# Kernel tuning notes

Measured on AMD Instinct MI355X. Metric: run time of the kernel, lower is better.

The kernel has to match this reference:

```python
import jax, jax.numpy as jnp
import numpy as np

NSTEPS = 20
ALPHA, BETA = 0.9, 0.85


def setup_inputs() -> dict:
    key = jax.random.key(0)
    ks = jax.random.split(key, 12)
    B, T, D_in, K, OUT = 64, NSTEPS, 16384, 25, 2
    dims = [8192, 4096, 2048]      # floor(dim/factor) per layer, factor=2
    prev = [16384, 8192, 4096]     # fan-in width each layer gathers from
    std = (2.0 / K) ** 0.5
    inp = {"x": jax.random.normal(ks[0], (B, T, D_in), jnp.float32)}
    for i, (d, p) in enumerate(zip(dims, prev)):
        inp[f"W{i}"] = jax.random.normal(ks[1 + i], (d, K), jnp.float32) * std
        inp[f"b{i}"] = jnp.zeros((1, d), jnp.float32)
        inp[f"knn{i}"] = jax.random.randint(ks[4 + i], (d, K), 0, p)
        inp[f"thr{i}"] = jax.random.uniform(ks[7 + i], (d,), jnp.float32)
    inp["Wfc"] = jax.random.normal(ks[10], (OUT, dims[-1]), jnp.float32) * dims[-1] ** -0.5
    inp["bfc"] = jnp.zeros((OUT,), jnp.float32)
    return inp


def reference(x, W0, b0, W1, b1, W2, b2, knn0, knn1, knn2,
              thr0, thr1, thr2, Wfc, bfc):
    # x: (B, T, D_in) -> scan over T
    Ws, bs = (W0, W1, W2), (b0, b1, b2)
    knns, thrs = (knn0, knn1, knn2), (thr0, thr1, thr2)
    n_layer = 3
    B = x.shape[0]
    xs = jnp.transpose(x, (1, 0, 2))  # (T, B, D_in)
    mems0 = tuple(jnp.zeros((B, w.shape[0]), x.dtype) for w in Ws)

    def step(mems, xt):
        h = xt
        new_mems, mem_recs, spk_recs = [], [], []
        for i in range(n_layer):
            g = h[:, knns[i]]                             # (B, dim_i, K) gather
            cur = jnp.einsum('bdk,dk->bd', g, Ws[i]) + bs[i]
            thr, mem_prev = thrs[i], mems[i]
            reset = (mem_prev > thr).astype(h.dtype)
            # NOTE: original code never writes the returned syn back, so the
            # synaptic state stays at zero init: syn = alpha*0 + cur = cur.
            syn = cur
            mem = BETA * mem_prev + syn - reset * thr
            spk = (mem - thr > 0).astype(h.dtype)
            if i == n_layer - 1:
                h = mem                 # last layer passes membrane forward
                new_mems.append(mem_prev)  # last-layer carry never updated
            else:
                h = spk
                new_mems.append(mem)
            mem_recs.append(mem)
            spk_recs.append(spk)
        angle = h @ Wfc.T + bfc
        return tuple(new_mems), (tuple(mem_recs), tuple(spk_recs), angle)

    _, (mem_rec, spk_rec, angles_all) = jax.lax.scan(step, mems0, xs)
    angles = angles_all[-1]  # original keeps only the last step's angle
    return (*mem_rec, *spk_rec, angles)
```

## Files before the change

kernel.cpp:

```cpp
#include <hip/hip_runtime.h>

#define NSTEPS 20
#define BATCH 64
#define D_IN 16384
#define KNN 25
#define BETA 0.85

#define D0 8192
#define D1 4096
#define D2 2048

#define NRT 24

__global__ void __launch_bounds__(256) transpose_x_kernel(
    const float* __restrict__ x, float* __restrict__ xT) {
  __shared__ float tile[64][65];
  const int t = blockIdx.y;
  const int d0 = blockIdx.x * 64;
  {
    const int dd = threadIdx.x & 63;
    const int bg = threadIdx.x >> 6;
#pragma unroll
    for (int i = 0; i < 16; ++i) {
      const int b = bg * 16 + i;
      tile[b][dd] = x[((size_t)b * NSTEPS + t) * D_IN + d0 + dd];
    }
  }
  __syncthreads();
  {
    const int b = threadIdx.x & 63;
    const int dg = threadIdx.x >> 6;
#pragma unroll
    for (int i = 0; i < 16; ++i) {
      const int d = dg * 16 + i;
      xT[((size_t)t * D_IN + d0 + d) * BATCH + b] = tile[b][d];
    }
  }
}

template <bool IS_U8>
__global__ void __launch_bounds__(512) cur_kernel(
    const void* __restrict__ src, size_t st_t, const float* __restrict__ W,
    const float* __restrict__ bias, const int* __restrict__ knn, int dn,
    int dchunk0, double* __restrict__ curbuf) {
  const int nb_d = dn >> 4;
  const int g = blockIdx.x & 7;
  const int q = blockIdx.x >> 3;
  const int r = q / nb_d;
  const int i = q - r * nb_d;
  const int t = r * 8 + g;
  if (t >= NSTEPS) return;

  const int lane = threadIdx.x & 63;
  const int wv = threadIdx.x >> 6;
  const int dl0 = i * 16 + wv * 2;

  double cc[2];
#pragma unroll
  for (int j = 0; j < 2; ++j) {
    const int dl = dl0 + j;
    const int dg = __builtin_amdgcn_readfirstlane(dchunk0 + dl);
    const int* kp = knn + (size_t)dg * KNN;
    const float* wp = W + (size_t)dg * KNN;
    double cur = (double)bias[dg];
    if (IS_U8) {
      const unsigned char* sp =
          (const unsigned char*)src + (size_t)t * st_t + lane;
#pragma unroll
      for (int k = 0; k < KNN; ++k) {
        const int idx = kp[k];
        cur += (double)wp[k] * (double)sp[(size_t)idx * BATCH];
      }
    } else {
      const float* sp = (const float*)src + (size_t)t * st_t + lane;
#pragma unroll
      for (int k = 0; k < KNN; ++k) {
        const int idx = kp[k];
        cur += (double)wp[k] * (double)sp[(size_t)idx * BATCH];
      }
    }
    cc[j] = cur;
  }
  double2 v;
  v.x = cc[0];
  v.y = cc[1];
  const size_t o =
      (((size_t)t * (dn >> 1) + (dl0 >> 1)) * BATCH + lane) * 2;
  *reinterpret_cast<double2*>(&curbuf[o]) = v;
}

__global__ void __launch_bounds__(512) scan_kernel(
    const double* __restrict__ curbuf, int dn, int dchunk0, int D,
    const float* __restrict__ thr, float* __restrict__ mem_rec,
    float* __restrict__ spk_rec, unsigned char* __restrict__ spkT) {
  __shared__ float s_mem[16][68];
  __shared__ float s_spk[16][68];
  const int dl0 = blockIdx.x * 16;
  const int lane = threadIdx.x & 63;
  const int wv = threadIdx.x >> 6;
  const int dbase = dl0 + wv * 2;

  double mem[2] = {0.0, 0.0};
  double thrv[2];
#pragma unroll
  for (int j = 0; j < 2; ++j) thrv[j] = (double)thr[dchunk0 + dbase + j];

  for (int t = 0; t < NSTEPS; ++t) {
    const double2 cc = *reinterpret_cast<const double2*>(
        &curbuf[(((size_t)t * (dn >> 1) + (dbase >> 1)) * BATCH + lane) * 2]);
#pragma unroll
    for (int j = 0; j < 2; ++j) {
      const int dl = dbase + j;
      const double cur = (j == 0) ? cc.x : cc.y;
      double m = mem[j];
      const double reset = (m > thrv[j]) ? thrv[j] : 0.0;
      m = BETA * m + cur - reset;
      mem[j] = m;
      const float spk = (m > thrv[j]) ? 1.0f : 0.0f;
      s_mem[wv * 2 + j][lane] = (float)m;
      s_spk[wv * 2 + j][lane] = spk;
      if (spkT)
        spkT[((size_t)t * D + dchunk0 + dl) * BATCH + lane] =
            (unsigned char)spk;
    }
    __syncthreads();
    {
      const int b = threadIdx.x & 63;
      const int q = threadIdx.x >> 6;
      const int dq = (q & 3) * 4;
      const float(*sp)[68] = (q < 4) ? s_mem : s_spk;
      float4 v;
      v.x = sp[dq + 0][b];
      v.y = sp[dq + 1][b];
      v.z = sp[dq + 2][b];
      v.w = sp[dq + 3][b];
      float* dst = (q < 4) ? mem_rec : spk_rec;
      const size_t o = ((size_t)t * BATCH + b) * D + dchunk0 + dl0 + dq;
      *reinterpret_cast<float4*>(&dst[o]) = v;
    }
    __syncthreads();
  }
}

template <bool IS_U8, bool CARRY>
__global__ void __launch_bounds__(512) layer_scan_kernel(
    const void* __restrict__ src, size_t st_t, size_t st_b, size_t st_idx,
    const float* __restrict__ W, const float* __restrict__ bias,
    const int* __restrict__ knn, const float* __restrict__ thr, int D,
    float* __restrict__ mem_rec, float* __restrict__ spk_rec,
    unsigned char* __restrict__ spkT) {
  __shared__ float s_mem[16][68];
  __shared__ float s_spk[16][68];
  const int d0 = blockIdx.x * 16;
  const int lane = threadIdx.x & 63;
  const int wv = threadIdx.x >> 6;
  const int dbase = d0 + wv * 2;

  double mem[2] = {0.0, 0.0};
  double thrv[2], bsv[2];
#pragma unroll
  for (int j = 0; j < 2; ++j) {
    thrv[j] = (double)thr[dbase + j];
    bsv[j] = (double)bias[dbase + j];
  }

  const int t_lo = CARRY ? 0 : (int)blockIdx.y;
  const int t_hi = CARRY ? NSTEPS : (int)blockIdx.y + 1;

  for (int t = t_lo; t < t_hi; ++t) {
#pragma unroll
    for (int j = 0; j < 2; ++j) {
      const int d = dbase + j;
      const int* kp = knn + (size_t)d * KNN;
      const float* wp = W + (size_t)d * KNN;
      const size_t base = (size_t)t * st_t + (size_t)lane * st_b;
      double cur = bsv[j];
#pragma unroll
      for (int k = 0; k < KNN; ++k) {
        const int idx = kp[k];
        if (IS_U8) {
          const unsigned char s =
              ((const unsigned char*)src)[base + (size_t)idx * st_idx];
          cur += (double)wp[k] * (double)s;
        } else {
          const float g = ((const float*)src)[base + (size_t)idx * st_idx];
          cur += (double)wp[k] * (double)g;
        }
      }
      double m = CARRY ? mem[j] : 0.0;
      const double reset = (m > thrv[j]) ? thrv[j] : 0.0;
      m = BETA * m + cur - reset;
      mem[j] = m;
      const float spk = (m > thrv[j]) ? 1.0f : 0.0f;
      s_mem[wv * 2 + j][lane] = (float)m;
      s_spk[wv * 2 + j][lane] = spk;
      if (spkT) spkT[((size_t)t * D + d) * BATCH + lane] = (unsigned char)spk;
    }
    __syncthreads();
    {
      const int b = threadIdx.x & 63;
      const int q = threadIdx.x >> 6;
      const int dq = (q & 3) * 4;
      const float(*sp)[68] = (q < 4) ? s_mem : s_spk;
      float4 v;
      v.x = sp[dq + 0][b];
      v.y = sp[dq + 1][b];
      v.z = sp[dq + 2][b];
      v.w = sp[dq + 3][b];
      float* dst = (q < 4) ? mem_rec : spk_rec;
      const size_t o = ((size_t)t * BATCH + b) * D + d0 + dq;
      *reinterpret_cast<float4*>(&dst[o]) = v;
    }
    __syncthreads();
  }
}

__global__ void __launch_bounds__(64) fc_kernel(
    const float* __restrict__ mem2, const float* __restrict__ Wfc,
    const float* __restrict__ bfc, float* __restrict__ angles) {
  const int b = blockIdx.x;
  const float* h = mem2 + ((size_t)(NSTEPS - 1) * BATCH + b) * D2;
  double a0 = 0.0, a1 = 0.0;
  for (int d = threadIdx.x; d < D2; d += 64) {
    const double m = (double)h[d];
    a0 += m * (double)Wfc[d];
    a1 += m * (double)Wfc[D2 + d];
  }
#pragma unroll
  for (int off = 32; off > 0; off >>= 1) {
    a0 += __shfl_down(a0, off);
    a1 += __shfl_down(a1, off);
  }
  if (threadIdx.x == 0) {
    angles[(size_t)b * 2 + 0] = (float)(a0 + (double)bfc[0]);
    angles[(size_t)b * 2 + 1] = (float)(a1 + (double)bfc[1]);
  }
}

extern "C" void kernel_launch(void* const* d_in, const int* in_sizes, int n_in,
                              void* d_out, int out_size, void* d_ws,
                              size_t ws_size, hipStream_t stream) {
  const float* x = (const float*)d_in[0];
  const float* W0 = (const float*)d_in[1];
  const float* b0 = (const float*)d_in[2];
  const int* knn0 = (const int*)d_in[3];
  const float* thr0 = (const float*)d_in[4];
  const float* W1 = (const float*)d_in[5];
  const float* b1 = (const float*)d_in[6];
  const int* knn1 = (const int*)d_in[7];
  const float* thr1 = (const float*)d_in[8];
  const float* W2 = (const float*)d_in[9];
  const float* b2 = (const float*)d_in[10];
  const int* knn2 = (const int*)d_in[11];
  const float* thr2 = (const float*)d_in[12];
  const float* Wfc = (const float*)d_in[13];
  const float* bfc = (const float*)d_in[14];

  float* out = (float*)d_out;
  float* mem_rec0 = out;
  float* mem_rec1 = mem_rec0 + (size_t)NSTEPS * BATCH * D0;
  float* mem_rec2 = mem_rec1 + (size_t)NSTEPS * BATCH * D1;
  float* spk_rec0 = mem_rec2 + (size_t)NSTEPS * BATCH * D2;
  float* spk_rec1 = spk_rec0 + (size_t)NSTEPS * BATCH * D0;
  float* spk_rec2 = spk_rec1 + (size_t)NSTEPS * BATCH * D1;
  float* angles = spk_rec2 + (size_t)NSTEPS * BATCH * D2;

  const size_t xT_bytes = (size_t)NSTEPS * D_IN * BATCH * sizeof(float);
  const size_t s0_bytes = (size_t)NSTEPS * D0 * BATCH;
  const size_t s1_bytes = (size_t)NSTEPS * D1 * BATCH;
  const size_t base_bytes = xT_bytes + s0_bytes + s1_bytes;

  const bool planA = ws_size >= base_bytes;
  const bool planB = !planA && ws_size >= s0_bytes + s1_bytes;

  size_t leftover = (ws_size > base_bytes) ? ws_size - base_bytes : 0;
  int Dc = (int)((leftover / ((size_t)NSTEPS * BATCH * 8)) & ~(size_t)15);
  if (Dc > D0) Dc = D0;
  const bool planT = planA && Dc >= 512;

  const dim3 blk(512);

  if (planT) {
    float* xT = (float*)d_ws;
    unsigned char* spk0T = (unsigned char*)d_ws + xT_bytes;
    unsigned char* spk1T = spk0T + s0_bytes;
    double* curbuf = (double*)((char*)d_ws + base_bytes);

    transpose_x_kernel<<<dim3(D_IN / 64, NSTEPS), 256, 0, stream>>>(x, xT);

    for (int c0 = 0; c0 < D0; c0 += Dc) {
      const int dn = (D0 - c0 < Dc) ? (D0 - c0) : Dc;
      cur_kernel<false><<<dim3(NRT * (dn / 16)), blk, 0, stream>>>(
          xT, (size_t)D_IN * BATCH, W0, b0, knn0, dn, c0, curbuf);
      scan_kernel<<<dim3(dn / 16), blk, 0, stream>>>(
          curbuf, dn, c0, D0, thr0, mem_rec0, spk_rec0, spk0T);
    }
    for (int c0 = 0; c0 < D1; c0 += Dc) {
      const int dn = (D1 - c0 < Dc) ? (D1 - c0) : Dc;
      cur_kernel<true><<<dim3(NRT * (dn / 16)), blk, 0, stream>>>(
          spk0T, (size_t)D0 * BATCH, W1, b1, knn1, dn, c0, curbuf);
      scan_kernel<<<dim3(dn / 16), blk, 0, stream>>>(
          curbuf, dn, c0, D1, thr1, mem_rec1, spk_rec1, spk1T);
    }
    layer_scan_kernel<true, false><<<dim3(D2 / 16, NSTEPS), blk, 0, stream>>>(
        spk1T, (size_t)D1 * BATCH, 1, BATCH, W2, b2, knn2, thr2, D2, mem_rec2,
        spk_rec2, nullptr);
  } else if (planA) {
    float* xT = (float*)d_ws;
    unsigned char* spk0T = (unsigned char*)d_ws + xT_bytes;
    unsigned char* spk1T = spk0T + s0_bytes;

    transpose_x_kernel<<<dim3(D_IN / 64, NSTEPS), 256, 0, stream>>>(x, xT);
    layer_scan_kernel<false, true><<<dim3(D0 / 16), blk, 0, stream>>>(
        xT, (size_t)D_IN * BATCH, 1, BATCH, W0, b0, knn0, thr0, D0, mem_rec0,
        spk_rec0, spk0T);
    layer_scan_kernel<true, true><<<dim3(D1 / 16), blk, 0, stream>>>(
        spk0T, (size_t)D0 * BATCH, 1, BATCH, W1, b1, knn1, thr1, D1, mem_rec1,
        spk_rec1, spk1T);
    layer_scan_kernel<true, false><<<dim3(D2 / 16, NSTEPS), blk, 0, stream>>>(
        spk1T, (size_t)D1 * BATCH, 1, BATCH, W2, b2, knn2, thr2, D2, mem_rec2,
        spk_rec2, nullptr);
  } else if (planB) {
    unsigned char* spk0T = (unsigned char*)d_ws;
    unsigned char* spk1T = spk0T + s0_bytes;

    layer_scan_kernel<false, true><<<dim3(D0 / 16), blk, 0, stream>>>(
        x, (size_t)D_IN, (size_t)NSTEPS * D_IN, 1, W0, b0, knn0, thr0, D0,
        mem_rec0, spk_rec0, spk0T);
    layer_scan_kernel<true, true><<<dim3(D1 / 16), blk, 0, stream>>>(
        spk0T, (size_t)D0 * BATCH, 1, BATCH, W1, b1, knn1, thr1, D1, mem_rec1,
        spk_rec1, spk1T);
    layer_scan_kernel<true, false><<<dim3(D2 / 16, NSTEPS), blk, 0, stream>>>(
        spk1T, (size_t)D1 * BATCH, 1, BATCH, W2, b2, knn2, thr2, D2, mem_rec2,
        spk_rec2, nullptr);
  } else {
    layer_scan_kernel<false, true><<<dim3(D0 / 16), blk, 0, stream>>>(
        x, (size_t)D_IN, (size_t)NSTEPS * D_IN, 1, W0, b0, knn0, thr0, D0,
        mem_rec0, spk_rec0, nullptr);
    layer_scan_kernel<false, true><<<dim3(D1 / 16), blk, 0, stream>>>(
        spk_rec0, (size_t)BATCH * D0, (size_t)D0, 1, W1, b1, knn1, thr1, D1,
        mem_rec1, spk_rec1, nullptr);
    layer_scan_kernel<false, false><<<dim3(D2 / 16, NSTEPS), blk, 0, stream>>>(
        spk_rec1, (size_t)BATCH * D1, (size_t)D1, 1, W2, b2, knn2, thr2, D2,
        mem_rec2, spk_rec2, nullptr);
  }

  fc_kernel<<<dim3(BATCH), 64, 0, stream>>>(mem_rec2, Wfc, bfc, angles);
}
```

Baseline: 249.5 us.

## Compact cur_kernel grid mapping and shrink scan blocks with two-step batching

The cur_kernel grid no longer launches 24 time-slots per d-block, of which 4 exit immediately. It now packs exactly NSTEPS*nb_d work items into 8 contiguous XCD-style groups, so each group gets a contiguous run of (t, d-block) items. scan_kernel drops to 256 threads covering 8 neurons, which doubles its block count for better occupancy. Each iteration now handles two timesteps, halving the barrier count and issuing both curbuf loads up front. The trade-off is more shared-memory staging per iteration and a changed block-to-XCD locality pattern.

Result: slower. 277.4 us (+11.2%).

```diff
diff --git a/kernel.cpp b/kernel.cpp
--- a/kernel.cpp
+++ b/kernel.cpp
@@ -9,8 +9,6 @@
 #define D0 8192
 #define D1 4096
 #define D2 2048
-
-#define NRT 24
 
 __global__ void __launch_bounds__(256) transpose_x_kernel(
     const float* __restrict__ x, float* __restrict__ xT) {
@@ -43,13 +41,15 @@
     const void* __restrict__ src, size_t st_t, const float* __restrict__ W,
     const float* __restrict__ bias, const int* __restrict__ knn, int dn,
     int dchunk0, double* __restrict__ curbuf) {
-  const int nb_d = dn >> 4;
-  const int g = blockIdx.x & 7;
-  const int q = blockIdx.x >> 3;
-  const int r = q / nb_d;
-  const int i = q - r * nb_d;
-  const int t = r * 8 + g;
-  if (t >= NSTEPS) return;
+  const unsigned nb_d = (unsigned)dn >> 4;
+  const unsigned Wk = NSTEPS * nb_d;
+  const unsigned C = (Wk + 7u) >> 3;
+  const unsigned g = blockIdx.x & 7u;
+  const unsigned s = blockIdx.x >> 3;
+  const unsigned u = g * C + s;
+  if (s >= C || u >= Wk) return;
+  const int t = (int)(u / nb_d);
+  const int i = (int)(u - (unsigned)t * nb_d);
 
   const int lane = threadIdx.x & 63;
   const int wv = threadIdx.x >> 6;
@@ -84,18 +84,17 @@
   double2 v;
   v.x = cc[0];
   v.y = cc[1];
-  const size_t o =
-      (((size_t)t * (dn >> 1) + (dl0 >> 1)) * BATCH + lane) * 2;
+  const size_t o = (((size_t)t * (dn >> 1) + (dl0 >> 1)) * BATCH + lane) * 2;
   *reinterpret_cast<double2*>(&curbuf[o]) = v;
 }
 
-__global__ void __launch_bounds__(512) scan_kernel(
+__global__ void __launch_bounds__(256) scan_kernel(
     const double* __restrict__ curbuf, int dn, int dchunk0, int D,
     const float* __restrict__ thr, float* __restrict__ mem_rec,
     float* __restrict__ spk_rec, unsigned char* __restrict__ spkT) {
-  __shared__ float s_mem[16][68];
-  __shared__ float s_spk[16][68];
-  const int dl0 = blockIdx.x * 16;
+  __shared__ float s_mem[2][8][68];
+  __shared__ float s_spk[2][8][68];
+  const int dl0 = blockIdx.x * 8;
   const int lane = threadIdx.x & 63;
   const int wv = threadIdx.x >> 6;
   const int dbase = dl0 + wv * 2;
@@ -105,38 +104,50 @@
 #pragma unroll
   for (int j = 0; j < 2; ++j) thrv[j] = (double)thr[dchunk0 + dbase + j];
 
-  for (int t = 0; t < NSTEPS; ++t) {
-    const double2 cc = *reinterpret_cast<const double2*>(
-        &curbuf[(((size_t)t * (dn >> 1) + (dbase >> 1)) * BATCH + lane) * 2]);
-#pragma unroll
-    for (int j = 0; j < 2; ++j) {
-      const int dl = dbase + j;
-      const double cur = (j == 0) ? cc.x : cc.y;
-      double m = mem[j];
-      const double reset = (m > thrv[j]) ? thrv[j] : 0.0;
-      m = BETA * m + cur - reset;
-      mem[j] = m;
-      const float spk = (m > thrv[j]) ? 1.0f : 0.0f;
-      s_mem[wv * 2 + j][lane] = (float)m;
-      s_spk[wv * 2 + j][lane] = spk;
-      if (spkT)
-        spkT[((size_t)t * D + dchunk0 + dl) * BATCH + lane] =
-            (unsigned char)spk;
+  const size_t row = (size_t)(dn >> 1);
+  for (int t0 = 0; t0 < NSTEPS; t0 += 2) {
+    const double2 c0 = *reinterpret_cast<const double2*>(
+        &curbuf[(((size_t)t0 * row + (dbase >> 1)) * BATCH + lane) * 2]);
+    const double2 c1 = *reinterpret_cast<const double2*>(
+        &curbuf[(((size_t)(t0 + 1) * row + (dbase >> 1)) * BATCH + lane) * 2]);
+#pragma unroll
+    for (int tt = 0; tt < 2; ++tt) {
+      const double2 cc = tt ? c1 : c0;
+      const int t = t0 + tt;
+#pragma unroll
+      for (int j = 0; j < 2; ++j) {
+        const int dl = dbase + j;
+        const double cur = (j == 0) ? cc.x : cc.y;
+        double m = mem[j];
+        const double reset = (m > thrv[j]) ? thrv[j] : 0.0;
+        m = BETA * m + cur - reset;
+        mem[j] = m;
+        const float spk = (m > thrv[j]) ? 1.0f : 0.0f;
+        s_mem[tt][wv * 2 + j][lane] = (float)m;
+        s_spk[tt][wv * 2 + j][lane] = spk;
+        if (spkT)
+          spkT[((size_t)t * D + dchunk0 + dl) * BATCH + lane] =
+              (unsigned char)spk;
+      }
     }
     __syncthreads();
     {
       const int b = threadIdx.x & 63;
       const int q = threadIdx.x >> 6;
-      const int dq = (q & 3) * 4;
-      const float(*sp)[68] = (q < 4) ? s_mem : s_spk;
-      float4 v;
-      v.x = sp[dq + 0][b];
-      v.y = sp[dq + 1][b];
-      v.z = sp[dq + 2][b];
-      v.w = sp[dq + 3][b];
-      float* dst = (q < 4) ? mem_rec : spk_rec;
-      const size_t o = ((size_t)t * BATCH + b) * D + dchunk0 + dl0 + dq;
-      *reinterpret_cast<float4*>(&dst[o]) = v;
+      const int dq = (q & 1) * 4;
+      float* dst = (q < 2) ? mem_rec : spk_rec;
+#pragma unroll
+      for (int tt = 0; tt < 2; ++tt) {
+        const float(*sp)[68] = (q < 2) ? s_mem[tt] : s_spk[tt];
+        float4 v;
+        v.x = sp[dq + 0][b];
+        v.y = sp[dq + 1][b];
+        v.z = sp[dq + 2][b];
+        v.w = sp[dq + 3][b];
+        const size_t o =
+            ((size_t)(t0 + tt) * BATCH + b) * D + dchunk0 + dl0 + dq;
+        *reinterpret_cast<float4*>(&dst[o]) = v;
+      }
     }
     __syncthreads();
   }
@@ -290,16 +301,20 @@
 
     for (int c0 = 0; c0 < D0; c0 += Dc) {
       const int dn = (D0 - c0 < Dc) ? (D0 - c0) : Dc;
-      cur_kernel<false><<<dim3(NRT * (dn / 16)), blk, 0, stream>>>(
+      const unsigned Wk = NSTEPS * ((unsigned)dn >> 4);
+      const unsigned grid = 8u * ((Wk + 7u) >> 3);
+      cur_kernel<false><<<dim3(grid), blk, 0, stream>>>(
           xT, (size_t)D_IN * BATCH, W0, b0, knn0, dn, c0, curbuf);
-      scan_kernel<<<dim3(dn / 16), blk, 0, stream>>>(
+      scan_kernel<<<dim3(dn / 8), 256, 0, stream>>>(
           curbuf, dn, c0, D0, thr0, mem_rec0, spk_rec0, spk0T);
     }
     for (int c0 = 0; c0 < D1; c0 += Dc) {
       const int dn = (D1 - c0 < Dc) ? (D1 - c0) : Dc;
-      cur_kernel<true><<<dim3(NRT * (dn / 16)), blk, 0, stream>>>(
+      const unsigned Wk = NSTEPS * ((unsigned)dn >> 4);
+      const unsigned grid = 8u * ((Wk + 7u) >> 3);
+      cur_kernel<true><<<dim3(grid), blk, 0, stream>>>(
           spk0T, (size_t)D0 * BATCH, W1, b1, knn1, dn, c0, curbuf);
-      scan_kernel<<<dim3(dn / 16), blk, 0, stream>>>(
+      scan_kernel<<<dim3(dn / 8), 256, 0, stream>>>(
           curbuf, dn, c0, D1, thr1, mem_rec1, spk_rec1, spk1T);
     }
     layer_scan_kernel<true, false><<<dim3(D2 / 16, NSTEPS), blk, 0, stream>>>(
```
